# Kernel optimization log

Measured on AMD Instinct MI355X. Metric: run time of the kernel, lower is better.

## Reference

```python
import jax, jax.numpy as jnp
import numpy as np

N_NODES = 100000
N_EDGES = 1600000
NUM_FEATURES = 128
DIMS = [(NUM_FEATURES, 50), (50, 50), (50, 30), (30, 30), (30, 10), (10, 10), (10, 1)]


def setup_inputs() -> dict:
    key = jax.random.key(0)
    ks = jax.random.split(key, 4 + 2 * len(DIMS))
    inp = {
        "x": jax.random.normal(ks[0], (N_NODES, NUM_FEATURES), dtype=jnp.float32),
        "edge_index": jax.random.randint(ks[1], (2, N_EDGES), 0, N_NODES, dtype=jnp.int64) if jax.config.read("jax_enable_x64") else jax.random.randint(ks[1], (2, N_EDGES), 0, N_NODES, dtype=jnp.int32),
        "edge_weight": jax.random.uniform(ks[2], (N_EDGES,), dtype=jnp.float32),
    }
    for i, (fi, fo) in enumerate(DIMS):
        scale = 1.0 / np.sqrt(fi)
        inp[f"W{i+1}"] = jax.random.normal(ks[3 + 2 * i], (fi, fo), dtype=jnp.float32) * scale
        inp[f"b{i+1}"] = jax.random.normal(ks[4 + 2 * i], (fo,), dtype=jnp.float32) * 0.01
    return inp


def _gcn_norm(edge_index, edge_weight, n):
    # Add self-loops with weight 1, then symmetric normalization (PyG GCNConv).
    loops = jnp.arange(n)
    row = jnp.concatenate([edge_index[0], loops])
    col = jnp.concatenate([edge_index[1], loops])
    w = jnp.concatenate([edge_weight, jnp.ones((n,), edge_weight.dtype)])
    deg = jnp.zeros((n,), edge_weight.dtype).at[col].add(w)
    dinv = jnp.where(deg > 0, 1.0 / jnp.sqrt(deg), 0.0)
    norm = dinv[row] * w * dinv[col]
    return row, col, norm


def _gcn_conv(x, row, col, norm, W, b):
    h = x @ W                                # [N, out]
    msg = h[row] * norm[:, None]             # gather + edge scale [E+N, out]
    out = jnp.zeros_like(h).at[col].add(msg) # scatter-add
    return out + b


def _forward(x, edge_index, edge_weight, params):
    n = x.shape[0]
    row, col, norm = _gcn_norm(edge_index, edge_weight, n)  # shared across layers
    h = x
    n_layers = len(params)
    for i, (W, b) in enumerate(params):
        h = _gcn_conv(h, row, col, norm, W, b)
        if i < n_layers - 1:
            h = jax.nn.relu(h)
        # F.dropout treated as identity (eval mode) for a deterministic reference
    return h


def reference(x, edge_index, edge_weight, W1, b1, W2, b2, W3, b3, W4, b4, W5, b5, W6, b6, W7, b7):
    params = [(W1, b1), (W2, b2), (W3, b3), (W4, b4), (W5, b5), (W6, b6), (W7, b7)]
    return _forward(x, edge_index, edge_weight, params)
```

## Files before the change

### kernel.cpp

```cpp
#include <hip/hip_runtime.h>
#include <hip/hip_fp16.h>


static constexpr int NN = 100000;
static constexpr int NE = 1600000;
static constexpr int BKL = 9;
static constexpr int NBUK = (NN + 511) >> BKL;
static constexpr int EPT = 8;
static constexpr int EB = (NE + 2047) / 2048;


__global__ __launch_bounds__(256) void k_hist0(const int* __restrict__ col,
                                               int* __restrict__ counts) {
    __shared__ int lh[NBUK];
    for (int j = threadIdx.x; j < NBUK; j += 256) lh[j] = 0;
    __syncthreads();
    int base = blockIdx.x * 2048;
#pragma unroll
    for (int k = 0; k < EPT; ++k) {
        int e = base + k * 256 + threadIdx.x;
        if (e < NE) atomicAdd(&lh[col[e] >> BKL], 1);
    }
    __syncthreads();
    for (int j = threadIdx.x; j < NBUK; j += 256)
        counts[j * EB + blockIdx.x] = lh[j];
}


__global__ __launch_bounds__(256) void k_scanA(int* __restrict__ counts,
                                               int* __restrict__ btot) {
    __shared__ int lds[256];
    const int b = blockIdx.x;
    const int t = threadIdx.x;
    int* c = counts + (size_t)b * EB;
    constexpr int PER = (EB + 255) / 256;
    int v[PER];
    int s = 0;
#pragma unroll
    for (int k = 0; k < PER; ++k) {
        int idx = t * PER + k;
        v[k] = (idx < EB) ? c[idx] : 0;
        s += v[k];
    }
    lds[t] = s;
    __syncthreads();
    for (int off = 1; off < 256; off <<= 1) {
        int u = (t >= off) ? lds[t - off] : 0;
        __syncthreads();
        lds[t] += u;
        __syncthreads();
    }
    int run = lds[t] - s;
#pragma unroll
    for (int k = 0; k < PER; ++k) {
        int idx = t * PER + k;
        if (idx < EB) { c[idx] = run; run += v[k]; }
    }
    if (t == 255) btot[b] = lds[255];
}


__global__ void k_scanB(const int* __restrict__ btot, int* __restrict__ bstart) {
    __shared__ int lds[256];
    int t = threadIdx.x;
    int v = (t < NBUK) ? btot[t] : 0;
    lds[t] = v;
    __syncthreads();
    for (int off = 1; off < 256; off <<= 1) {
        int u = (t >= off) ? lds[t - off] : 0;
        __syncthreads();
        lds[t] += u;
        __syncthreads();
    }
    if (t < NBUK) bstart[t] = lds[t] - v;
    if (t == 0) bstart[NBUK] = NE;
}


__global__ __launch_bounds__(256) void k_A1(const int* __restrict__ row,
                                            const int* __restrict__ col,
                                            const float* __restrict__ ew,
                                            const int* __restrict__ counts,
                                            const int* __restrict__ bstart,
                                            int2* __restrict__ stg) {
    __shared__ int cur[NBUK];
    for (int j = threadIdx.x; j < NBUK; j += 256)
        cur[j] = bstart[j] + counts[j * EB + blockIdx.x];
    __syncthreads();
    int base = blockIdx.x * 2048;
#pragma unroll
    for (int k = 0; k < EPT; ++k) {
        int e = base + k * 256 + threadIdx.x;
        if (e < NE) {
            int c = col[e], r = row[e];
            int pos = atomicAdd(&cur[c >> BKL], 1);
            stg[pos] = make_int2(((c & 511) << 17) | r, __float_as_int(ew[e]));
        }
    }
}


__global__ __launch_bounds__(256) void k_bdeg(const int* __restrict__ bstart,
                                              const int2* __restrict__ stg,
                                              float* __restrict__ dinv) {
    __shared__ float sdeg[512];
    const int b = blockIdx.x;
    for (int j = threadIdx.x; j < 512; j += 256) sdeg[j] = 0.0f;
    __syncthreads();
    const int s = bstart[b], e = bstart[b + 1];
    for (int p = s + threadIdx.x; p < e; p += 256) {
        int2 rec = stg[p];
        atomicAdd(&sdeg[rec.x >> 17], __int_as_float(rec.y));
    }
    __syncthreads();
    for (int j = threadIdx.x; j < 512; j += 256) {
        int idx = (b << BKL) + j;
        if (idx < NN) dinv[idx] = rsqrtf(sdeg[j] + 1.0f);
    }
}


__global__ __launch_bounds__(512) void k_place(const int* __restrict__ bstart,
                                               const int2* __restrict__ stg,
                                               const float* __restrict__ dinv,
                                               int* __restrict__ offs,
                                               int2* __restrict__ csw) {
    __shared__ int lcnt[512];
    __shared__ int cur[512];
    const int b = blockIdx.x;
    const int t = threadIdx.x;
    lcnt[t] = 0;
    __syncthreads();
    const int s = bstart[b], e = bstart[b + 1];
    for (int p = s + t; p < e; p += 512)
        atomicAdd(&lcnt[stg[p].x >> 17], 1);
    __syncthreads();
    int v = lcnt[t];
    for (int off = 1; off < 512; off <<= 1) {
        int u = (t >= off) ? lcnt[t - off] : 0;
        __syncthreads();
        lcnt[t] += u;
        __syncthreads();
    }
    int excl = lcnt[t] - v;
    int idx = (b << BKL) + t;
    if (idx <= NN) offs[idx] = s + excl;
    cur[t] = s + excl;
    __syncthreads();
    for (int p = s + t; p < e; p += 512) {
        int2 rec = stg[p];
        int cl = rec.x >> 17;
        int r = rec.x & 0x1FFFF;
        float nw = dinv[r] * __int_as_float(rec.y) * dinv[(b << BKL) + cl];
        int slot = atomicAdd(&cur[cl], 1);
        csw[slot] = make_int2(r, __float_as_int(nw));
    }
}


typedef short s16x8 __attribute__((ext_vector_type(8)));
typedef float f32x4v __attribute__((ext_vector_type(4)));

static __device__ __forceinline__ unsigned short bf16rn(float f) {
    unsigned u = __float_as_uint(f);
    return (unsigned short)((u + 0x7FFFu + ((u >> 16) & 1u)) >> 16);
}

__global__ void k_wsplit(const float* __restrict__ W, short* __restrict__ wt) {
    const int t = threadIdx.x;
#pragma unroll
    for (int i = 0; i < 32; ++i) {
        const int li = t + 256 * i;
        const int c = li >> 7, k = li & 127;
        float f = (c < 50) ? W[k * 50 + c] : 0.f;
        unsigned short hb = bf16rn(f);
        float hf = __uint_as_float((unsigned)hb << 16);
        unsigned short lb = bf16rn(f - hf);
        const int off = c * 128 + (k ^ ((c & 7) << 3));
        wt[off] = (short)hb;
        wt[8192 + off] = (short)lb;
    }
}

__global__ __launch_bounds__(256, 4) void k_matmul_f(const float* __restrict__ X,
                                                     const short* __restrict__ wt,
                                                     __half* __restrict__ H) {
    __shared__ short lds[2 * 64 * 128];
    const int t = threadIdx.x;

    {
        const int4* src = (const int4*)wt;
        int4* dst = (int4*)lds;
#pragma unroll
        for (int j = 0; j < 8; ++j) dst[j * 256 + t] = src[j * 256 + t];
    }

    const int w = t >> 6;
    const int lane = t & 63;
    const int lr = lane & 15;
    const int kg = lane >> 4;
    const int row = blockIdx.x * 64 + 16 * w + lr;
    const float* xr = X + (size_t)(row < NN ? row : NN - 1) * 128 + kg * 8;

    float4 xa[4][2];
#pragma unroll
    for (int kb = 0; kb < 4; ++kb) {
        xa[kb][0] = *(const float4*)(xr + kb * 32);
        xa[kb][1] = *(const float4*)(xr + kb * 32 + 4);
    }

    __syncthreads();

    f32x4v acc[4];
#pragma unroll
    for (int ct = 0; ct < 4; ++ct) acc[ct] = (f32x4v){0.f, 0.f, 0.f, 0.f};

#pragma unroll
    for (int kb = 0; kb < 4; ++kb) {
        s16x8 ah, al;
        const unsigned* xu = (const unsigned*)&xa[kb][0];
#pragma unroll
        for (int e = 0; e < 8; ++e) {
            const unsigned u = xu[e];
            const float lo = __uint_as_float(u) - __uint_as_float(u & 0xFFFF0000u);
            ah[e] = (short)(u >> 16);
            al[e] = (short)(__float_as_uint(lo) >> 16);
        }
        const int kf = kb * 32 + kg * 8;
        s16x8 bh[4], bl[4];
#pragma unroll
        for (int ct = 0; ct < 4; ++ct) {
            const int bc = ct * 16 + lr;
            const int ko = bc * 128 + (kf ^ ((bc & 7) << 3));
            bh[ct] = *(const s16x8*)&lds[ko];
            bl[ct] = *(const s16x8*)&lds[8192 + ko];
        }
#pragma unroll
        for (int ct = 0; ct < 4; ++ct)
            acc[ct] = __builtin_amdgcn_mfma_f32_16x16x32_bf16(ah, bh[ct], acc[ct], 0, 0, 0);
#pragma unroll
        for (int ct = 0; ct < 4; ++ct)
            acc[ct] = __builtin_amdgcn_mfma_f32_16x16x32_bf16(ah, bl[ct], acc[ct], 0, 0, 0);
#pragma unroll
        for (int ct = 0; ct < 4; ++ct)
            acc[ct] = __builtin_amdgcn_mfma_f32_16x16x32_bf16(al, bh[ct], acc[ct], 0, 0, 0);
    }

    const int gr = blockIdx.x * 64 + 16 * w + kg * 4;
#pragma unroll
    for (int ct = 0; ct < 4; ++ct) {
        const int col = ct * 16 + lr;
        if (col < 50) {
#pragma unroll
            for (int rg = 0; rg < 4; ++rg) {
                const int orow = gr + rg;
                if (orow < NN)
                    H[(size_t)orow * 64 + col] = __float2half_rn(acc[ct][rg]);
            }
        }
    }
}


template <int FIN, int SX, int FOUT, int S, int NSPL>
__global__ __launch_bounds__(256, 2) void k_matmul_h(const __half* __restrict__ X,
                                                     const float* __restrict__ W,
                                                     __half* __restrict__ H) {
    constexpr int FC = FOUT / NSPL;
    constexpr int NCH = (FIN + 7) / 8;
    const int node = blockIdx.x * 256 + threadIdx.x;
    const int ch = blockIdx.y;
    if (node >= NN) return;
    const __half* xr = X + (size_t)node * SX;
    int4 raw[NCH];
#pragma unroll
    for (int c = 0; c < NCH; ++c) raw[c] = *(const int4*)(xr + 8 * c);
    float acc[FC];
#pragma unroll
    for (int j = 0; j < FC; ++j) acc[j] = 0.0f;
#pragma unroll
    for (int c = 0; c < NCH; ++c) {
        const __half2* hp = (const __half2*)&raw[c];
        const int lim = (FIN - 8 * c < 8) ? FIN - 8 * c : 8;
#pragma unroll
        for (int kk = 0; kk < 8; ++kk) {
            if (kk < lim) {
                __half2 pair = hp[kk >> 1];
                float xv = (kk & 1) ? __high2float(pair) : __low2float(pair);
                const float* wrow = W + (8 * c + kk) * FOUT + ch * FC;
#pragma unroll
                for (int j = 0; j < FC; ++j) acc[j] = fmaf(xv, wrow[j], acc[j]);
            }
        }
    }
    __half* hr = H + (size_t)node * S + ch * FC;
#pragma unroll
    for (int j = 0; j < FC; ++j) hr[j] = __float2half_rn(acc[j]);
}

__global__ void k_matmul_1h(const __half* __restrict__ X, const float* __restrict__ W,
                            float* __restrict__ H) {
    int i = blockIdx.x * blockDim.x + threadIdx.x;
    if (i >= NN) return;
    const __half* xr = X + (size_t)i * 16;
    int4 r0 = *(const int4*)xr;
    __half2 r1 = *(const __half2*)(xr + 8);
    const __half2* hp = (const __half2*)&r0;
    float acc = 0.0f;
#pragma unroll
    for (int q = 0; q < 4; ++q) {
        acc = fmaf(__low2float(hp[q]), W[2 * q], acc);
        acc = fmaf(__high2float(hp[q]), W[2 * q + 1], acc);
    }
    acc = fmaf(__low2float(r1), W[8], acc);
    acc = fmaf(__high2float(r1), W[9], acc);
    H[i] = acc;
}


static __device__ __forceinline__ int2 nt_load2(const int2* p) {
    unsigned long long raw = __builtin_nontemporal_load((const unsigned long long*)p);
    return make_int2((int)(raw & 0xFFFFFFFFull), (int)(raw >> 32));
}

template <int F, int SH, int SA, int LPN, bool RELU>
__global__ __launch_bounds__(256) void k_agg2(const int* __restrict__ offs,
                                              const int2* __restrict__ csw,
                                              const __half2* __restrict__ H,
                                              const float* __restrict__ dinv,
                                              const float* __restrict__ b,
                                              __half* __restrict__ O) {
    constexpr int R = F / 2;
    int t = blockIdx.x * blockDim.x + threadIdx.x;
    int g = t / LPN;
    int f = t - g * LPN;
    if (g >= NN) return;
    const int q0 = 4 * f;
    if (q0 >= R) return;
    int p = offs[g];
    const int pe = offs[g + 1];
    const int pl = pe - 1;

    float2 acc[4];
#pragma unroll
    for (int c = 0; c < 4; ++c) acc[c] = make_float2(0.f, 0.f);

    for (; p < pe; p += 4) {
        int2 e[4];
#pragma unroll
        for (int i = 0; i < 4; ++i) e[i] = nt_load2(csw + min(p + i, pl));
        __half2 h[4][4];
#pragma unroll
        for (int i = 0; i < 4; ++i)
            *(int4*)h[i] = *(const int4*)(H + (size_t)e[i].x * SH + q0);
#pragma unroll
        for (int i = 0; i < 4; ++i) {
            float w = (p + i < pe) ? __int_as_float(e[i].y) : 0.0f;
#pragma unroll
            for (int c = 0; c < 4; ++c) {
                acc[c].x = fmaf(__low2float(h[i][c]), w, acc[c].x);
                acc[c].y = fmaf(__high2float(h[i][c]), w, acc[c].y);
            }
        }
    }

    float di = dinv[g];
    float d2 = di * di;
    __half2 hs[4];
    *(int4*)hs = *(const int4*)(H + (size_t)g * SH + q0);
    __half2* orow = (__half2*)(O + (size_t)g * SA) + q0;
#pragma unroll
    for (int c = 0; c < 4; ++c) {
        if (q0 + c < R) {
            float vx = acc[c].x + fmaf(__low2float(hs[c]), d2, b[2 * (q0 + c)]);
            float vy = acc[c].y + fmaf(__high2float(hs[c]), d2, b[2 * (q0 + c) + 1]);
            if (RELU) { vx = fmaxf(vx, 0.f); vy = fmaxf(vy, 0.f); }
            orow[c] = __floats2half2_rn(vx, vy);
        }
    }
}

__global__ void k_agg1(const int* __restrict__ offs, const int2* __restrict__ csw,
                       const float* __restrict__ H, const float* __restrict__ dinv,
                       const float* __restrict__ b, float* __restrict__ O) {
    int g = blockIdx.x * blockDim.x + threadIdx.x;
    if (g >= NN) return;
    int p = offs[g];
    const int pe = offs[g + 1];
    const int pl = pe - 1;
    float a0 = 0.f, a1 = 0.f, a2 = 0.f, a3 = 0.f;
    for (; p < pe; p += 4) {
        int2 e0 = nt_load2(csw + min(p, pl)),     e1 = nt_load2(csw + min(p + 1, pl));
        int2 e2 = nt_load2(csw + min(p + 2, pl)), e3 = nt_load2(csw + min(p + 3, pl));
        float w0 = (p < pe)     ? __int_as_float(e0.y) : 0.f;
        float w1 = (p + 1 < pe) ? __int_as_float(e1.y) : 0.f;
        float w2 = (p + 2 < pe) ? __int_as_float(e2.y) : 0.f;
        float w3 = (p + 3 < pe) ? __int_as_float(e3.y) : 0.f;
        a0 = fmaf(H[e0.x], w0, a0);
        a1 = fmaf(H[e1.x], w1, a1);
        a2 = fmaf(H[e2.x], w2, a2);
        a3 = fmaf(H[e3.x], w3, a3);
    }
    float di = dinv[g];
    O[g] = ((a0 + a1) + (a2 + a3)) + fmaf(H[g], di * di, b[0]);
}


static inline size_t alignup(size_t x) { return (x + 255) & ~(size_t)255; }

extern "C" void kernel_launch(void* const* d_in, const int* in_sizes, int n_in,
                              void* d_out, int out_size, void* d_ws, size_t ws_size,
                              hipStream_t stream) {
    const float* x  = (const float*)d_in[0];
    const int*   ei = (const int*)d_in[1];
    const float* ew = (const float*)d_in[2];
    const float* Wp[7];
    const float* Bp[7];
    for (int l = 0; l < 7; ++l) {
        Wp[l] = (const float*)d_in[3 + 2 * l];
        Bp[l] = (const float*)d_in[4 + 2 * l];
    }
    const int* row = ei;
    const int* col = ei + NE;

    char* ws = (char*)d_ws;
    float* dinv  = (float*)ws;  ws += alignup((size_t)NN * 4);
    char*  Hb    = ws;          ws += alignup((size_t)NN * 64 * 2);
    char*  Aa    = ws;          ws += alignup((size_t)NN * 64 * 2);
    char*  Ab    = ws;          ws += alignup((size_t)NN * 64 * 2);
    int*   offs  = (int*)ws;    ws += alignup((size_t)(NN + 1) * 4);
    int*   counts= (int*)ws;    ws += alignup((size_t)NBUK * EB * 4);
    int*   btot  = (int*)ws;    ws += alignup((size_t)NBUK * 4);
    int*   bstart= (int*)ws;    ws += alignup((size_t)(NBUK + 1) * 4);
    int2*  stg   = (int2*)ws;   ws += alignup((size_t)NE * 8);
    int2*  csw   = (int2*)ws;   ws += alignup((size_t)NE * 8);
    short* wt    = (short*)ws;  ws += alignup((size_t)2 * 64 * 128 * 2);

    const int gN = (NN + 255) / 256;
    const int gM = (NN + 63) / 64;

    k_wsplit<<<1, 256, 0, stream>>>(Wp[0], wt);
    k_hist0<<<EB, 256, 0, stream>>>(col, counts);
    k_scanA<<<NBUK, 256, 0, stream>>>(counts, btot);
    k_scanB<<<1, 256, 0, stream>>>(btot, bstart);
    k_A1<<<EB, 256, 0, stream>>>(row, col, ew, counts, bstart, stg);
    k_bdeg<<<NBUK, 256, 0, stream>>>(bstart, stg, dinv);
    k_place<<<NBUK, 512, 0, stream>>>(bstart, stg, dinv, offs, csw);

#define AGG(FOUT, S, LPN, RELU, OUT, LIDX)                                                  \
    k_agg2<FOUT, (S) / 2, S, LPN, RELU>                                                     \
        <<<((size_t)NN * (LPN) + 255) / 256, 256, 0, stream>>>(                             \
            offs, csw, (const __half2*)Hb, dinv, Bp[LIDX], (__half*)(OUT))

    k_matmul_f<<<gM, 256, 0, stream>>>(x, wt, (__half*)Hb);
    AGG(50, 64, 8, true, Aa, 0);
    k_matmul_h<50, 64, 50, 64, 2><<<dim3(gN, 2), 256, 0, stream>>>((const __half*)Aa, Wp[1], (__half*)Hb);
    AGG(50, 64, 8, true, Ab, 1);
    k_matmul_h<50, 64, 30, 32, 2><<<dim3(gN, 2), 256, 0, stream>>>((const __half*)Ab, Wp[2], (__half*)Hb);
    AGG(30, 32, 4, true, Aa, 2);
    k_matmul_h<30, 32, 30, 32, 2><<<dim3(gN, 2), 256, 0, stream>>>((const __half*)Aa, Wp[3], (__half*)Hb);
    AGG(30, 32, 4, true, Ab, 3);
    k_matmul_h<30, 32, 10, 16, 1><<<dim3(gN, 1), 256, 0, stream>>>((const __half*)Ab, Wp[4], (__half*)Hb);
    AGG(10, 16, 2, true, Aa, 4);
    k_matmul_h<10, 16, 10, 16, 1><<<dim3(gN, 1), 256, 0, stream>>>((const __half*)Aa, Wp[5], (__half*)Hb);
    AGG(10, 16, 2, true, Ab, 5);
#undef AGG

    k_matmul_1h<<<gN, 256, 0, stream>>>((const __half*)Ab, Wp[6], (float*)Hb);
    k_agg1<<<gN, 256, 0, stream>>>(offs, csw, (const float*)Hb, dinv, Bp[6],
                                   (float*)d_out);
}
```

Measured before the change: 457.7 us.

## Move hidden-layer dense transforms onto f16 MFMA with pre-split weights

```diff
diff --git a/kernel.cpp b/kernel.cpp
--- a/kernel.cpp
+++ b/kernel.cpp
@@ -160,19 +160,43 @@
 
 typedef short s16x8 __attribute__((ext_vector_type(8)));
 typedef float f32x4v __attribute__((ext_vector_type(4)));
+typedef _Float16 f16x8 __attribute__((ext_vector_type(8)));
 
 static __device__ __forceinline__ unsigned short bf16rn(float f) {
     unsigned u = __float_as_uint(f);
     return (unsigned short)((u + 0x7FFFu + ((u >> 16) & 1u)) >> 16);
 }
 
-__global__ void k_wsplit(const float* __restrict__ W, short* __restrict__ wt) {
+static constexpr int WT2 = 16384;
+static constexpr int WT3 = WT2 + 9216;
+static constexpr int WT4 = WT3 + 4608;
+static constexpr int WT5 = WT4 + 2560;
+static constexpr int WT_TOT = WT5 + 1280;
+
+static __device__ __forceinline__ void prep_f16(const float* __restrict__ W,
+                                                int FIN, int FOUT, int KP,
+                                                int PITCH, int NCT,
+                                                short* __restrict__ dst, int t) {
+    const int WCNT = NCT * 16 * PITCH;
+    for (int li = t; li < NCT * 16 * KP; li += 256) {
+        const int c = li / KP, k = li - c * KP;
+        float f = (c < FOUT && k < FIN) ? W[k * FOUT + c] : 0.f;
+        __half hh = __float2half_rn(f);
+        __half hl = __float2half_rn(f - __half2float(hh));
+        dst[c * PITCH + k] = __half_as_short(hh);
+        dst[WCNT + c * PITCH + k] = __half_as_short(hl);
+    }
+}
+
+__global__ void k_wprep(const float* __restrict__ W0, const float* __restrict__ W1,
+                        const float* __restrict__ W2, const float* __restrict__ W3,
+                        const float* __restrict__ W4, short* __restrict__ wt) {
     const int t = threadIdx.x;
 #pragma unroll
     for (int i = 0; i < 32; ++i) {
         const int li = t + 256 * i;
         const int c = li >> 7, k = li & 127;
-        float f = (c < 50) ? W[k * 50 + c] : 0.f;
+        float f = (c < 50) ? W0[k * 50 + c] : 0.f;
         unsigned short hb = bf16rn(f);
         float hf = __uint_as_float((unsigned)hb << 16);
         unsigned short lb = bf16rn(f - hf);
@@ -180,21 +204,24 @@
         wt[off] = (short)hb;
         wt[8192 + off] = (short)lb;
     }
-}
+    prep_f16(W1, 50, 50, 64, 72, 4, wt + WT2, t);
+    prep_f16(W2, 50, 30, 64, 72, 2, wt + WT3, t);
+    prep_f16(W3, 30, 30, 32, 40, 2, wt + WT4, t);
+    prep_f16(W4, 30, 10, 32, 40, 1, wt + WT5, t);
+}
+
 
 __global__ __launch_bounds__(256, 4) void k_matmul_f(const float* __restrict__ X,
                                                      const short* __restrict__ wt,
                                                      __half* __restrict__ H) {
     __shared__ short lds[2 * 64 * 128];
     const int t = threadIdx.x;
-
     {
         const int4* src = (const int4*)wt;
         int4* dst = (int4*)lds;
 #pragma unroll
         for (int j = 0; j < 8; ++j) dst[j * 256 + t] = src[j * 256 + t];
     }
-
     const int w = t >> 6;
     const int lane = t & 63;
     const int lr = lane & 15;
@@ -208,7 +235,6 @@
         xa[kb][0] = *(const float4*)(xr + kb * 32);
         xa[kb][1] = *(const float4*)(xr + kb * 32 + 4);
     }
-
     __syncthreads();
 
     f32x4v acc[4];
@@ -256,6 +282,66 @@
                 const int orow = gr + rg;
                 if (orow < NN)
                     H[(size_t)orow * 64 + col] = __float2half_rn(acc[ct][rg]);
+            }
+        }
+    }
+}
+
+
+template <int FIN, int KP, int PITCH, int SX, int FOUT, int NCT, int S>
+__global__ __launch_bounds__(256, 4) void k_matmul_fh(const __half* __restrict__ X,
+                                                      const short* __restrict__ wt,
+                                                      __half* __restrict__ H) {
+    constexpr int NKB = KP / 32;
+    constexpr int WCNT = NCT * 16 * PITCH;
+    __shared__ short lds[2 * WCNT];
+    const int t = threadIdx.x;
+    {
+        const int4* src = (const int4*)wt;
+        int4* dst = (int4*)lds;
+        constexpr int NI = (2 * WCNT) / 8;
+        for (int j = t; j < NI; j += 256) dst[j] = src[j];
+    }
+    const int w = t >> 6;
+    const int lane = t & 63;
+    const int lr = lane & 15;
+    const int kg = lane >> 4;
+    const int row = blockIdx.x * 64 + 16 * w + lr;
+    const __half* xr = X + (size_t)(row < NN ? row : NN - 1) * SX + kg * 8;
+
+    int4 xa[NKB];
+#pragma unroll
+    for (int kb = 0; kb < NKB; ++kb) xa[kb] = *(const int4*)(xr + kb * 32);
+    __syncthreads();
+
+    f32x4v acc[NCT];
+#pragma unroll
+    for (int ct = 0; ct < NCT; ++ct) acc[ct] = (f32x4v){0.f, 0.f, 0.f, 0.f};
+
+#pragma unroll
+    for (int kb = 0; kb < NKB; ++kb) {
+        f16x8 a = *(const f16x8*)&xa[kb];
+        const int kf = kb * 32 + kg * 8;
+#pragma unroll
+        for (int ct = 0; ct < NCT; ++ct) {
+            const int c = ct * 16 + lr;
+            f16x8 bh = *(const f16x8*)&lds[c * PITCH + kf];
+            f16x8 bl = *(const f16x8*)&lds[WCNT + c * PITCH + kf];
+            acc[ct] = __builtin_amdgcn_mfma_f32_16x16x32_f16(a, bh, acc[ct], 0, 0, 0);
+            acc[ct] = __builtin_amdgcn_mfma_f32_16x16x32_f16(a, bl, acc[ct], 0, 0, 0);
+        }
+    }
+
+    const int gr = blockIdx.x * 64 + 16 * w + kg * 4;
+#pragma unroll
+    for (int ct = 0; ct < NCT; ++ct) {
+        const int col = ct * 16 + lr;
+        if (col < FOUT) {
+#pragma unroll
+            for (int rg = 0; rg < 4; ++rg) {
+                const int orow = gr + rg;
+                if (orow < NN)
+                    H[(size_t)orow * S + col] = __float2half_rn(acc[ct][rg]);
             }
         }
     }
@@ -336,7 +422,14 @@
     int f = t - g * LPN;
     if (g >= NN) return;
     const int q0 = 4 * f;
-    if (q0 >= R) return;
+    __half2* orow = (__half2*)(O + (size_t)g * SA) + q0;
+    if (q0 >= R) {
+        const __half2 z = __floats2half2_rn(0.f, 0.f);
+#pragma unroll
+        for (int c = 0; c < 4; ++c)
+            if (q0 + c < SA / 2) orow[c] = z;
+        return;
+    }
     int p = offs[g];
     const int pe = offs[g + 1];
     const int pl = pe - 1;
@@ -368,7 +461,6 @@
     float d2 = di * di;
     __half2 hs[4];
     *(int4*)hs = *(const int4*)(H + (size_t)g * SH + q0);
-    __half2* orow = (__half2*)(O + (size_t)g * SA) + q0;
 #pragma unroll
     for (int c = 0; c < 4; ++c) {
         if (q0 + c < R) {
@@ -376,6 +468,8 @@
             float vy = acc[c].y + fmaf(__high2float(hs[c]), d2, b[2 * (q0 + c) + 1]);
             if (RELU) { vx = fmaxf(vx, 0.f); vy = fmaxf(vy, 0.f); }
             orow[c] = __floats2half2_rn(vx, vy);
+        } else if (q0 + c < SA / 2) {
+            orow[c] = __floats2half2_rn(0.f, 0.f);
         }
     }
 }
@@ -434,12 +528,12 @@
     int*   bstart= (int*)ws;    ws += alignup((size_t)(NBUK + 1) * 4);
     int2*  stg   = (int2*)ws;   ws += alignup((size_t)NE * 8);
     int2*  csw   = (int2*)ws;   ws += alignup((size_t)NE * 8);
-    short* wt    = (short*)ws;  ws += alignup((size_t)2 * 64 * 128 * 2);
+    short* wt    = (short*)ws;  ws += alignup((size_t)WT_TOT * 2);
 
     const int gN = (NN + 255) / 256;
     const int gM = (NN + 63) / 64;
 
-    k_wsplit<<<1, 256, 0, stream>>>(Wp[0], wt);
+    k_wprep<<<1, 256, 0, stream>>>(Wp[0], Wp[1], Wp[2], Wp[3], Wp[4], wt);
     k_hist0<<<EB, 256, 0, stream>>>(col, counts);
     k_scanA<<<NBUK, 256, 0, stream>>>(counts, btot);
     k_scanB<<<1, 256, 0, stream>>>(btot, bstart);
@@ -454,13 +548,13 @@
 
     k_matmul_f<<<gM, 256, 0, stream>>>(x, wt, (__half*)Hb);
     AGG(50, 64, 8, true, Aa, 0);
-    k_matmul_h<50, 64, 50, 64, 2><<<dim3(gN, 2), 256, 0, stream>>>((const __half*)Aa, Wp[1], (__half*)Hb);
+    k_matmul_fh<50, 64, 72, 64, 50, 4, 64><<<gM, 256, 0, stream>>>((const __half*)Aa, wt + WT2, (__half*)Hb);
     AGG(50, 64, 8, true, Ab, 1);
-    k_matmul_h<50, 64, 30, 32, 2><<<dim3(gN, 2), 256, 0, stream>>>((const __half*)Ab, Wp[2], (__half*)Hb);
+    k_matmul_fh<50, 64, 72, 64, 30, 2, 32><<<gM, 256, 0, stream>>>((const __half*)Ab, wt + WT3, (__half*)Hb);
     AGG(30, 32, 4, true, Aa, 2);
-    k_matmul_h<30, 32, 30, 32, 2><<<dim3(gN, 2), 256, 0, stream>>>((const __half*)Aa, Wp[3], (__half*)Hb);
+    k_matmul_fh<30, 32, 40, 32, 30, 2, 32><<<gM, 256, 0, stream>>>((const __half*)Aa, wt + WT4, (__half*)Hb);
     AGG(30, 32, 4, true, Ab, 3);
-    k_matmul_h<30, 32, 10, 16, 1><<<dim3(gN, 1), 256, 0, stream>>>((const __half*)Ab, Wp[4], (__half*)Hb);
+    k_matmul_fh<30, 32, 40, 32, 10, 1, 16><<<gM, 256, 0, stream>>>((const __half*)Ab, wt + WT5, (__half*)Hb);
     AGG(10, 16, 2, true, Aa, 4);
     k_matmul_h<10, 16, 10, 16, 1><<<dim3(gN, 1), 256, 0, stream>>>((const __half*)Aa, Wp[5], (__half*)Hb);
     AGG(10, 16, 2, true, Ab, 5);
```

After: 442.0 us. 3.4% less time.
